# Performance work log

Measured on AMD Instinct MI355X. Metric: run time of the kernel, lower is better.

## Reference

```python
import jax, jax.numpy as jnp
from jax import lax
import numpy as np

N = 16384          # number of input points
RATIO = 0.25       # sampling_ratio
S = int(N * RATIO) # number of FPS seeds
K = 32             # neighborhood_size
EMB = 384          # embedding_size
EPS = 1e-5         # batch-norm eps


def setup_inputs() -> dict:
    key = jax.random.key(0)
    ks = jax.random.split(key, 8)
    d = {}
    d['pos'] = jax.random.normal(ks[0], (N, 3), dtype=jnp.float32)
    d['batch'] = jnp.zeros((N,), dtype=jnp.int64)
    # mlp_1 = MLP([3,128,256]): Lin(3->128), BN(128), ReLU, Lin(128->256) (plain last)
    d['w1a'] = jax.random.normal(ks[1], (3, 128), dtype=jnp.float32) * 0.5
    d['b1a'] = jnp.zeros((128,), jnp.float32)
    d['g1'] = jnp.ones((128,), jnp.float32)
    d['be1'] = jnp.zeros((128,), jnp.float32)
    d['mu1'] = jnp.zeros((128,), jnp.float32)
    d['var1'] = jnp.ones((128,), jnp.float32)
    d['w1b'] = jax.random.normal(ks[2], (128, 256), dtype=jnp.float32) * 0.08
    d['b1b'] = jnp.zeros((256,), jnp.float32)
    # mlp_2 = MLP([512,512,EMB]): Lin(512->512), BN(512), ReLU, Lin(512->EMB)
    d['w2a'] = jax.random.normal(ks[3], (512, 512), dtype=jnp.float32) * 0.04
    d['b2a'] = jnp.zeros((512,), jnp.float32)
    d['g2'] = jnp.ones((512,), jnp.float32)
    d['be2'] = jnp.zeros((512,), jnp.float32)
    d['mu2'] = jnp.zeros((512,), jnp.float32)
    d['var2'] = jnp.ones((512,), jnp.float32)
    d['w2b'] = jax.random.normal(ks[4], (512, EMB), dtype=jnp.float32) * 0.04
    d['b2b'] = jnp.zeros((EMB,), jnp.float32)
    return d


def _fps(pos, num_samples):
    # farthest point sampling, deterministic start at index 0 (random_start=False)
    n = pos.shape[0]
    def step(carry, _):
        dists, last = carry
        d = jnp.sum((pos - pos[last]) ** 2, axis=-1)
        dists = jnp.minimum(dists, d)
        nxt = jnp.argmax(dists)
        return (dists, nxt), nxt
    init = (jnp.full((n,), jnp.inf, dtype=pos.dtype), jnp.asarray(0, jnp.int32))
    _, idx = lax.scan(step, init, None, length=num_samples - 1)
    return jnp.concatenate([jnp.zeros((1,), jnp.int32), idx.astype(jnp.int32)])


def _mlp(x, wa, ba, g, be, mu, var, wb, bb):
    h = x @ wa + ba
    h = (h - mu) * lax.rsqrt(var + EPS) * g + be  # BatchNorm (eval stats)
    h = jax.nn.relu(h)
    return h @ wb + bb


def reference(pos, batch, w1a, b1a, g1, be1, mu1, var1, w1b, b1b,
              w2a, b2a, g2, be2, mu2, var2, w2b, b2b):
    del batch  # single graph (all zeros)
    seed_idx = _fps(pos, S)
    seeds = pos[seed_idx]                                   # (S, 3)
    # brute-force KNN: squared distances seeds->points
    d2 = (jnp.sum(seeds * seeds, -1)[:, None]
          + jnp.sum(pos * pos, -1)[None, :]
          - 2.0 * seeds @ pos.T)                            # (S, N)
    _, nbr = lax.top_k(-d2, K)                              # (S, K) ascending distance
    rel = pos[nbr] - seeds[:, None, :]                      # (S, K, 3) = pos_j - pos_i
    h = _mlp(rel.reshape(-1, 3), w1a, b1a, g1, be1, mu1, var1, w1b, b1b)
    h = h.reshape(S, K, 256)
    hmax = jnp.max(h, axis=1, keepdims=True)                # neighborhood max-pool
    m = jnp.concatenate([jnp.broadcast_to(hmax, (S, K, 256)), h], axis=-1)  # (S,K,512)
    out = _mlp(m.reshape(-1, 512), w2a, b2a, g2, be2, mu2, var2, w2b, b2b)
    out = out.reshape(S, K, EMB)
    # aggr='max' over each seed's K contiguous edges
    return jnp.max(out, axis=1)                             # (S, EMB)
```

## Files before the change

### kernel.cpp

```cpp
#include <hip/hip_runtime.h>

#define NPTS 16384
#define NSEED 4096
#define KNB 32
#define TOTROWS (NSEED*KNB)
#define FPS_T 512

typedef float f32x4 __attribute__((ext_vector_type(4)));
typedef short s16x8 __attribute__((ext_vector_type(8)));

__device__ __forceinline__ unsigned short f2bf(float f){
    unsigned int u = __float_as_uint(f);
    u = (u + 0x7FFFu + ((u >> 16) & 1u)) >> 16;
    return (unsigned short)u;
}

__global__ void prep_kernel(const float* __restrict__ pos,
                            const float* __restrict__ w1b,
                            const float* __restrict__ w2a,
                            const float* __restrict__ w2b,
                            float* __restrict__ pp,
                            unsigned short* __restrict__ w1bT,
                            unsigned short* __restrict__ w2aT,
                            unsigned short* __restrict__ w2bT){
    int i = blockIdx.x*blockDim.x + threadIdx.x;
    int stride = gridDim.x*blockDim.x;
    for (int j=i;j<NPTS;j+=stride){
        float x=pos[3*j], y=pos[3*j+1], z=pos[3*j+2];
        pp[j] = __fadd_rn(__fadd_rn(__fmul_rn(x,x),__fmul_rn(y,y)),__fmul_rn(z,z));
    }
    for (int e=i;e<256*128;e+=stride){ int n=e>>7,k=e&127; w1bT[e]=f2bf(w1b[k*256+n]); }
    for (int e=i;e<512*512;e+=stride){ int n=e>>9,k=e&511; w2aT[e]=f2bf(w2a[k*512+n]); }
    for (int e=i;e<384*512;e+=stride){ int n=e>>9,k=e&511; w2bT[e]=f2bf(w2b[k*384+n]); }
}

#define REP32(X) X(0)X(1)X(2)X(3)X(4)X(5)X(6)X(7)X(8)X(9)X(10)X(11)X(12)X(13)X(14)X(15)X(16)X(17)X(18)X(19)X(20)X(21)X(22)X(23)X(24)X(25)X(26)X(27)X(28)X(29)X(30)X(31)

__global__ __launch_bounds__(FPS_T,2) void fps_kernel(const float* __restrict__ pos,
                                                      int* __restrict__ seed_idx,
                                                      float* __restrict__ seeds){
    __shared__ float2 slot[2][FPS_T/64];
    const int t = threadIdx.x;
    const int lane = t&63, wv = t>>6;
#define FPS_DECL(r) float px##r,py##r,pz##r,dd##r;
    REP32(FPS_DECL)
#define FPS_INIT(r) { const int j=t+((r)<<9); px##r=pos[3*j]; py##r=pos[3*j+1]; pz##r=pos[3*j+2]; dd##r=__builtin_inff(); }
    REP32(FPS_INIT)
    if (t==0){
        seed_idx[0]=0;
        seeds[0]=pos[0]; seeds[1]=pos[1]; seeds[2]=pos[2];
    }
    float lx=pos[0], ly=pos[1], lz=pos[2];
    for (int i=1;i<NSEED;i++){
        float best=-1.0f; int bj=0x7fffffff;
#define FPS_DIST(r) { \
        float dx=__fsub_rn(px##r,lx); \
        float dy=__fsub_rn(py##r,ly); \
        float dz=__fsub_rn(pz##r,lz); \
        float d=__fadd_rn(__fadd_rn(__fmul_rn(dx,dx),__fmul_rn(dy,dy)),__fmul_rn(dz,dz)); \
        float nd=fminf(dd##r,d); \
        dd##r=nd; \
        if (nd>best){ best=nd; bj=t+((r)<<9); } }
        REP32(FPS_DIST)
#pragma unroll
        for (int off=1;off<64;off<<=1){
            float ov=__shfl_xor(best,off);
            int   oj=__shfl_xor(bj,off);
            if (ov>best || (ov==best && oj<bj)){ best=ov; bj=oj; }
        }
        const int par=i&1;
        if (lane==0) slot[par][wv]=make_float2(best,(float)bj);
        __syncthreads();
        float gv=slot[par][0].x, gjf=slot[par][0].y;
#pragma unroll
        for (int w=1;w<FPS_T/64;w++){
            float2 s=slot[par][w];
            if (s.x>gv || (s.x==gv && s.y<gjf)){ gv=s.x; gjf=s.y; }
        }
        const int jwin=(int)gjf;
        lx=pos[3*jwin]; ly=pos[3*jwin+1]; lz=pos[3*jwin+2];
        if (t==0){ seed_idx[i]=jwin; seeds[3*i]=lx; seeds[3*i+1]=ly; seeds[3*i+2]=lz; }
    }
}

__global__ __launch_bounds__(256) void knn_kernel(const float* __restrict__ pos,
                                                  const float* __restrict__ pp,
                                                  const float* __restrict__ seeds,
                                                  float* __restrict__ rel){
    const int lane = threadIdx.x & 63;
    const int s = blockIdx.x*4 + (threadIdx.x>>6);
    const float sx=seeds[3*s], sy=seeds[3*s+1], sz=seeds[3*s+2];
    const float ss = __fadd_rn(__fadd_rn(__fmul_rn(sx,sx),__fmul_rn(sy,sy)),__fmul_rn(sz,sz));
    const float s2x=__fmul_rn(2.0f,sx), s2y=__fmul_rn(2.0f,sy), s2z=__fmul_rn(2.0f,sz);
    float lv=__builtin_inff(); int li=0;
    float curmax=__builtin_inff();
    for (int c=0;c<NPTS/64;c++){
        const int j=(c<<6)+lane;
        float x=pos[3*j], y=pos[3*j+1], z=pos[3*j+2];
        float dot=__fmul_rn(s2x,x);
        dot=fmaf(s2y,y,dot);
        dot=fmaf(s2z,z,dot);
        float d2=__fsub_rn(__fadd_rn(ss,pp[j]),dot);
        unsigned long long m=__ballot(d2<curmax);
        while (m){
            int src=__builtin_ctzll(m);
            m&=m-1;
            float bv=__shfl(d2,src);
            if (bv<curmax){
                int bjj=(c<<6)+src;
                float upv=__shfl_up(lv,1);
                int   upi=__shfl_up(li,1);
                bool keep=(lv<=bv);
                bool upless=(upv<=bv)||(lane==0);
                lv = keep?lv:(upless?bv:upv);
                li = keep?li:(upless?bjj:upi);
                curmax=__shfl(lv,31);
            }
        }
    }
    if (lane<KNB){
        int nb=li;
        float* o=&rel[(size_t)(s*KNB+lane)*3];
        o[0]=__fsub_rn(pos[3*nb],sx);
        o[1]=__fsub_rn(pos[3*nb+1],sy);
        o[2]=__fsub_rn(pos[3*nb+2],sz);
    }
}

__global__ __launch_bounds__(256,2) void mlp1_kernel(const float* __restrict__ rel,
    const float* __restrict__ w1a, const float* __restrict__ b1a,
    const float* __restrict__ g1, const float* __restrict__ be1,
    const float* __restrict__ mu1, const float* __restrict__ var1,
    const unsigned short* __restrict__ w1bT, const float* __restrict__ b1b,
    unsigned short* __restrict__ hbuf, unsigned short* __restrict__ hmaxb,
    int rowBase){
    __shared__ __align__(16) unsigned short h1[256][136];
    const int t=threadIdx.x;
    const int lrow = blockIdx.x*256 + t;
    const int grow = rowBase + lrow;
    {
        const float x0=rel[3*(size_t)grow], x1=rel[3*(size_t)grow+1], x2=rel[3*(size_t)grow+2];
#pragma unroll 4
        for (int c=0;c<128;c++){
            float v=__fmul_rn(x0,w1a[c]);
            v=fmaf(x1,w1a[128+c],v);
            v=fmaf(x2,w1a[256+c],v);
            v=__fadd_rn(v,b1a[c]);
            float rs=1.0f/__fsqrt_rn(__fadd_rn(var1[c],1e-5f));
            v=__fadd_rn(__fmul_rn(__fmul_rn(__fsub_rn(v,mu1[c]),rs),g1[c]),be1[c]);
            v=fmaxf(v,0.0f);
            h1[t][c]=f2bf(v);
        }
    }
    __syncthreads();
    const int lane=t&63, wv=t>>6;
    const int m=lane&15, kg=lane>>4;
    const int r0=wv*64;
#pragma unroll 1
    for (int nc=0;nc<4;nc++){
        f32x4 acc[4][4];
#pragma unroll
        for (int nt=0;nt<4;nt++){
            float bi=b1b[nc*64+nt*16+m];
            f32x4 vv={bi,bi,bi,bi};
#pragma unroll
            for (int mt=0;mt<4;mt++) acc[mt][nt]=vv;
        }
#pragma unroll
        for (int ks=0;ks<4;ks++){
            s16x8 a[4],b[4];
#pragma unroll
            for (int mt=0;mt<4;mt++)
                a[mt]=*(const s16x8*)&h1[r0+mt*16+m][ks*32+kg*8];
#pragma unroll
            for (int nt=0;nt<4;nt++)
                b[nt]=*(const s16x8*)&w1bT[(size_t)(nc*64+nt*16+m)*128 + ks*32+kg*8];
#pragma unroll
            for (int mt=0;mt<4;mt++)
#pragma unroll
                for (int nt=0;nt<4;nt++)
                    acc[mt][nt]=__builtin_amdgcn_mfma_f32_16x16x32_bf16(a[mt],b[nt],acc[mt][nt],0,0,0);
        }
#pragma unroll
        for (int nt=0;nt<4;nt++){
            float pA=-__builtin_inff(), pB=-__builtin_inff();
#pragma unroll
            for (int mt=0;mt<4;mt++){
#pragma unroll
                for (int rg=0;rg<4;rg++){
                    float v=acc[mt][nt][rg];
                    int lr = blockIdx.x*256 + r0 + mt*16 + kg*4 + rg;
                    hbuf[(size_t)lr*256 + nc*64+nt*16+m]=f2bf(v);
                    if (mt<2) pA=fmaxf(pA,v); else pB=fmaxf(pB,v);
                }
            }
            pA=fmaxf(pA,__shfl_xor(pA,16)); pA=fmaxf(pA,__shfl_xor(pA,32));
            pB=fmaxf(pB,__shfl_xor(pB,16)); pB=fmaxf(pB,__shfl_xor(pB,32));
            if (lane<16){
                int sA=(rowBase + blockIdx.x*256 + r0)>>5;
                hmaxb[(size_t)sA*256 + nc*64+nt*16+m]=f2bf(pA);
                hmaxb[(size_t)(sA+1)*256 + nc*64+nt*16+m]=f2bf(pB);
            }
        }
    }
}

__global__ __launch_bounds__(256,2) void mlp2_kernel(const unsigned short* __restrict__ hbuf,
    const unsigned short* __restrict__ hmaxb, const unsigned short* __restrict__ w2aT,
    const float* __restrict__ b2a, const float* __restrict__ g2, const float* __restrict__ be2,
    const float* __restrict__ mu2, const float* __restrict__ var2,
    unsigned short* __restrict__ gbuf, int rowBase){
    __shared__ __align__(16) unsigned short at[64][520];
    const int t=threadIdx.x;
    const int br = blockIdx.x*64;
    {
        const int lr=t>>2, q=t&3;
        const s16x8* srcH=(const s16x8*)&hbuf[((size_t)(br+lr))*256 + q*64];
        s16x8* dstH=(s16x8*)&at[lr][256+q*64];
        const int sd=(rowBase+br+lr)>>5;
        const s16x8* srcM=(const s16x8*)&hmaxb[(size_t)sd*256 + q*64];
        s16x8* dstM=(s16x8*)&at[lr][q*64];
#pragma unroll
        for (int u=0;u<8;u++){ dstH[u]=srcH[u]; dstM[u]=srcM[u]; }
    }
    __syncthreads();
    const int lane=t&63, wv=t>>6;
    const int m=lane&15, kg=lane>>4;
    const int n0=wv*128;
    f32x4 acc[4][8];
#pragma unroll
    for (int nt=0;nt<8;nt++){
        float bi=b2a[n0+nt*16+m];
        f32x4 vv={bi,bi,bi,bi};
#pragma unroll
        for (int mt=0;mt<4;mt++) acc[mt][nt]=vv;
    }
#pragma unroll 2
    for (int ks=0;ks<16;ks++){
        s16x8 a[4],b[8];
#pragma unroll
        for (int mt=0;mt<4;mt++) a[mt]=*(const s16x8*)&at[mt*16+m][ks*32+kg*8];
#pragma unroll
        for (int nt=0;nt<8;nt++) b[nt]=*(const s16x8*)&w2aT[(size_t)(n0+nt*16+m)*512 + ks*32+kg*8];
#pragma unroll
        for (int mt=0;mt<4;mt++)
#pragma unroll
            for (int nt=0;nt<8;nt++)
                acc[mt][nt]=__builtin_amdgcn_mfma_f32_16x16x32_bf16(a[mt],b[nt],acc[mt][nt],0,0,0);
    }
#pragma unroll
    for (int nt=0;nt<8;nt++){
        const int n=n0+nt*16+m;
        const float rs=1.0f/__fsqrt_rn(__fadd_rn(var2[n],1e-5f));
        const float mu=mu2[n], gg=g2[n], bb=be2[n];
#pragma unroll
        for (int mt=0;mt<4;mt++){
#pragma unroll
            for (int rg=0;rg<4;rg++){
                float v=acc[mt][nt][rg];
                v=__fadd_rn(__fmul_rn(__fmul_rn(__fsub_rn(v,mu),rs),gg),bb);
                v=fmaxf(v,0.0f);
                const int lr=br+mt*16+kg*4+rg;
                gbuf[(size_t)lr*512+n]=f2bf(v);
            }
        }
    }
}

__global__ __launch_bounds__(256,2) void mlp3_kernel(const unsigned short* __restrict__ gbuf,
    const unsigned short* __restrict__ w2bT, const float* __restrict__ b2b,
    float* __restrict__ outp, int rowBase){
    __shared__ __align__(16) unsigned short at[64][520];
    const int t=threadIdx.x;
    const int br=blockIdx.x*64;
    {
        const int lr=t>>2,q=t&3;
        const s16x8* src=(const s16x8*)&gbuf[((size_t)(br+lr))*512+q*128];
        s16x8* dst=(s16x8*)&at[lr][q*128];
#pragma unroll
        for (int u=0;u<16;u++) dst[u]=src[u];
    }
    __syncthreads();
    const int lane=t&63, wv=t>>6;
    const int m=lane&15, kg=lane>>4;
    const int n0=wv*96;
    f32x4 acc[4][6];
#pragma unroll
    for (int nt=0;nt<6;nt++){
        float bi=b2b[n0+nt*16+m];
        f32x4 vv={bi,bi,bi,bi};
#pragma unroll
        for (int mt=0;mt<4;mt++) acc[mt][nt]=vv;
    }
#pragma unroll 2
    for (int ks=0;ks<16;ks++){
        s16x8 a[4],b[6];
#pragma unroll
        for (int mt=0;mt<4;mt++) a[mt]=*(const s16x8*)&at[mt*16+m][ks*32+kg*8];
#pragma unroll
        for (int nt=0;nt<6;nt++) b[nt]=*(const s16x8*)&w2bT[(size_t)(n0+nt*16+m)*512+ks*32+kg*8];
#pragma unroll
        for (int mt=0;mt<4;mt++)
#pragma unroll
            for (int nt=0;nt<6;nt++)
                acc[mt][nt]=__builtin_amdgcn_mfma_f32_16x16x32_bf16(a[mt],b[nt],acc[mt][nt],0,0,0);
    }
    const int sA=(rowBase+br)>>5;
#pragma unroll
    for (int nt=0;nt<6;nt++){
        float pA=-__builtin_inff(), pB=-__builtin_inff();
#pragma unroll
        for (int mt=0;mt<4;mt++){
#pragma unroll
            for (int rg=0;rg<4;rg++){
                float v=acc[mt][nt][rg];
                if (mt<2) pA=fmaxf(pA,v); else pB=fmaxf(pB,v);
            }
        }
        pA=fmaxf(pA,__shfl_xor(pA,16)); pA=fmaxf(pA,__shfl_xor(pA,32));
        pB=fmaxf(pB,__shfl_xor(pB,16)); pB=fmaxf(pB,__shfl_xor(pB,32));
        if (lane<16){
            outp[(size_t)sA*384 + n0+nt*16+m]=pA;
            outp[(size_t)(sA+1)*384 + n0+nt*16+m]=pB;
        }
    }
}

extern "C" void kernel_launch(void* const* d_in, const int* in_sizes, int n_in,
                              void* d_out, int out_size, void* d_ws, size_t ws_size,
                              hipStream_t stream) {
    const float* pos =(const float*)d_in[0];
    const float* w1a =(const float*)d_in[2];
    const float* b1a =(const float*)d_in[3];
    const float* g1  =(const float*)d_in[4];
    const float* be1 =(const float*)d_in[5];
    const float* mu1 =(const float*)d_in[6];
    const float* var1=(const float*)d_in[7];
    const float* w1b =(const float*)d_in[8];
    const float* b1b =(const float*)d_in[9];
    const float* w2a =(const float*)d_in[10];
    const float* b2a =(const float*)d_in[11];
    const float* g2  =(const float*)d_in[12];
    const float* be2 =(const float*)d_in[13];
    const float* mu2 =(const float*)d_in[14];
    const float* var2=(const float*)d_in[15];
    const float* w2b =(const float*)d_in[16];
    const float* b2b =(const float*)d_in[17];

    char* base=(char*)d_ws;
    size_t off=0;
    auto alloc=[&](size_t bytes)->void*{
        void* p=base+off; off=(off+bytes+255)&~(size_t)255; return p;
    };
    int*   seed_idx=(int*)  alloc((size_t)NSEED*4);
    float* seeds   =(float*)alloc((size_t)NSEED*3*4);
    float* pp      =(float*)alloc((size_t)NPTS*4);
    float* rel     =(float*)alloc((size_t)TOTROWS*3*4);
    unsigned short* hmaxb=(unsigned short*)alloc((size_t)NSEED*256*2);
    unsigned short* w1bT =(unsigned short*)alloc((size_t)256*128*2);
    unsigned short* w2aT =(unsigned short*)alloc((size_t)512*512*2);
    unsigned short* w2bT =(unsigned short*)alloc((size_t)384*512*2);
    size_t fixed=off;

    int nch=512;
    for (int c=1;c<=512;c*=2){
        size_t need=fixed + (size_t)(TOTROWS/c)*(256*2 + 512*2) + 1024;
        if (need<=ws_size){ nch=c; break; }
    }
    const int chunkRows=TOTROWS/nch;
    unsigned short* hbuf=(unsigned short*)alloc((size_t)chunkRows*256*2);
    unsigned short* gbuf=(unsigned short*)alloc((size_t)chunkRows*512*2);

    prep_kernel<<<256,256,0,stream>>>(pos,w1b,w2a,w2b,pp,w1bT,w2aT,w2bT);
    fps_kernel<<<1,FPS_T,0,stream>>>(pos,seed_idx,seeds);
    knn_kernel<<<NSEED/4,256,0,stream>>>(pos,pp,seeds,rel);
    for (int c=0;c<nch;c++){
        const int rowBase=c*chunkRows;
        mlp1_kernel<<<chunkRows/256,256,0,stream>>>(rel,w1a,b1a,g1,be1,mu1,var1,w1bT,b1b,hbuf,hmaxb,rowBase);
        mlp2_kernel<<<chunkRows/64,256,0,stream>>>(hbuf,hmaxb,w2aT,b2a,g2,be2,mu2,var2,gbuf,rowBase);
        mlp3_kernel<<<chunkRows/64,256,0,stream>>>(gbuf,w2bT,b2b,(float*)d_out,rowBase);
    }
}
```

Before: 8.871 ms.

## Double FPS threads and stream point coords from LDS and global instead of registers

The single-block farthest point sampling kernel now uses 1024 threads with 16 points each instead of 512 threads with 32. x/y coordinates are staged in a 128KB shared-memory array, and z is read each iteration from a separate global array written by the prep kernel. Only the running min-distances stay in registers. This trades register residency for more parallel lanes on the serial FPS loop, but adds LDS and global loads every iteration and a larger cross-wave reduction.

New measurement: 10.23 ms. 15.3% more time.

```diff
diff --git a/kernel.cpp b/kernel.cpp
--- a/kernel.cpp
+++ b/kernel.cpp
@@ -4,7 +4,8 @@
 #define NSEED 4096
 #define KNB 32
 #define TOTROWS (NSEED*KNB)
-#define FPS_T 512
+#define FPS_T 1024
+#define FPS_R (NPTS/FPS_T)
 
 typedef float f32x4 __attribute__((ext_vector_type(4)));
 typedef short s16x8 __attribute__((ext_vector_type(8)));
@@ -20,6 +21,7 @@
                             const float* __restrict__ w2a,
                             const float* __restrict__ w2b,
                             float* __restrict__ pp,
+                            float* __restrict__ zs,
                             unsigned short* __restrict__ w1bT,
                             unsigned short* __restrict__ w2aT,
                             unsigned short* __restrict__ w2bT){
@@ -28,40 +30,50 @@
     for (int j=i;j<NPTS;j+=stride){
         float x=pos[3*j], y=pos[3*j+1], z=pos[3*j+2];
         pp[j] = __fadd_rn(__fadd_rn(__fmul_rn(x,x),__fmul_rn(y,y)),__fmul_rn(z,z));
+        zs[j] = z;
     }
     for (int e=i;e<256*128;e+=stride){ int n=e>>7,k=e&127; w1bT[e]=f2bf(w1b[k*256+n]); }
     for (int e=i;e<512*512;e+=stride){ int n=e>>9,k=e&511; w2aT[e]=f2bf(w2a[k*512+n]); }
     for (int e=i;e<384*512;e+=stride){ int n=e>>9,k=e&511; w2bT[e]=f2bf(w2b[k*384+n]); }
 }
 
-#define REP32(X) X(0)X(1)X(2)X(3)X(4)X(5)X(6)X(7)X(8)X(9)X(10)X(11)X(12)X(13)X(14)X(15)X(16)X(17)X(18)X(19)X(20)X(21)X(22)X(23)X(24)X(25)X(26)X(27)X(28)X(29)X(30)X(31)
-
-__global__ __launch_bounds__(FPS_T,2) void fps_kernel(const float* __restrict__ pos,
-                                                      int* __restrict__ seed_idx,
-                                                      float* __restrict__ seeds){
+#define REP16(X) X(0)X(1)X(2)X(3)X(4)X(5)X(6)X(7)X(8)X(9)X(10)X(11)X(12)X(13)X(14)X(15)
+
+__global__ __launch_bounds__(FPS_T) void fps_kernel(const float* __restrict__ pos,
+                                                    const float* __restrict__ zs,
+                                                    int* __restrict__ seed_idx,
+                                                    float* __restrict__ seeds){
+    __shared__ float2 xy[NPTS];
     __shared__ float2 slot[2][FPS_T/64];
     const int t = threadIdx.x;
     const int lane = t&63, wv = t>>6;
-#define FPS_DECL(r) float px##r,py##r,pz##r,dd##r;
-    REP32(FPS_DECL)
-#define FPS_INIT(r) { const int j=t+((r)<<9); px##r=pos[3*j]; py##r=pos[3*j+1]; pz##r=pos[3*j+2]; dd##r=__builtin_inff(); }
-    REP32(FPS_INIT)
+#pragma unroll
+    for (int r=0;r<FPS_R;r++){
+        const int j = t + (r<<10);
+        xy[j] = make_float2(pos[3*j], pos[3*j+1]);
+    }
+#define FPS_DECL(r) float dd##r = __builtin_inff();
+    REP16(FPS_DECL)
     if (t==0){
         seed_idx[0]=0;
         seeds[0]=pos[0]; seeds[1]=pos[1]; seeds[2]=pos[2];
     }
     float lx=pos[0], ly=pos[1], lz=pos[2];
+    __syncthreads();
     for (int i=1;i<NSEED;i++){
         float best=-1.0f; int bj=0x7fffffff;
 #define FPS_DIST(r) { \
-        float dx=__fsub_rn(px##r,lx); \
-        float dy=__fsub_rn(py##r,ly); \
-        float dz=__fsub_rn(pz##r,lz); \
+        const int j=t+((r)<<10); \
+        float2 v=xy[j]; \
+        float z=zs[j]; \
+        float dx=__fsub_rn(v.x,lx); \
+        float dy=__fsub_rn(v.y,ly); \
+        float dz=__fsub_rn(z,lz); \
         float d=__fadd_rn(__fadd_rn(__fmul_rn(dx,dx),__fmul_rn(dy,dy)),__fmul_rn(dz,dz)); \
         float nd=fminf(dd##r,d); \
         dd##r=nd; \
-        if (nd>best){ best=nd; bj=t+((r)<<9); } }
-        REP32(FPS_DIST)
+        if (nd>best){ best=nd; bj=j; } }
+        REP16(FPS_DIST)
 #pragma unroll
         for (int off=1;off<64;off<<=1){
             float ov=__shfl_xor(best,off);
@@ -78,7 +90,9 @@
             if (s.x>gv || (s.x==gv && s.y<gjf)){ gv=s.x; gjf=s.y; }
         }
         const int jwin=(int)gjf;
-        lx=pos[3*jwin]; ly=pos[3*jwin+1]; lz=pos[3*jwin+2];
+        float2 wxy = xy[jwin];
+        lz = zs[jwin];
+        lx = wxy.x; ly = wxy.y;
         if (t==0){ seed_idx[i]=jwin; seeds[3*i]=lx; seeds[3*i+1]=ly; seeds[3*i+2]=lz; }
     }
 }
@@ -355,6 +369,7 @@
     int*   seed_idx=(int*)  alloc((size_t)NSEED*4);
     float* seeds   =(float*)alloc((size_t)NSEED*3*4);
     float* pp      =(float*)alloc((size_t)NPTS*4);
+    float* zs      =(float*)alloc((size_t)NPTS*4);
     float* rel     =(float*)alloc((size_t)TOTROWS*3*4);
     unsigned short* hmaxb=(unsigned short*)alloc((size_t)NSEED*256*2);
     unsigned short* w1bT =(unsigned short*)alloc((size_t)256*128*2);
@@ -371,8 +386,8 @@
     unsigned short* hbuf=(unsigned short*)alloc((size_t)chunkRows*256*2);
     unsigned short* gbuf=(unsigned short*)alloc((size_t)chunkRows*512*2);
 
-    prep_kernel<<<256,256,0,stream>>>(pos,w1b,w2a,w2b,pp,w1bT,w2aT,w2bT);
-    fps_kernel<<<1,FPS_T,0,stream>>>(pos,seed_idx,seeds);
+    prep_kernel<<<256,256,0,stream>>>(pos,w1b,w2a,w2b,pp,zs,w1bT,w2aT,w2bT);
+    fps_kernel<<<1,FPS_T,0,stream>>>(pos,zs,seed_idx,seeds);
     knn_kernel<<<NSEED/4,256,0,stream>>>(pos,pp,seeds,rel);
     for (int c=0;c<nch;c++){
         const int rowBase=c*chunkRows;
```
